# Kernel optimization log

Hardware: AMD Instinct MI355X
Metric: run time of the kernel (lower is better)

The kernel has to match this reference:

```python
import jax, jax.numpy as jnp
import numpy as np

HID = 768
INNER = 1536   # hidden_size * expand_factor
NSTATE = 16
KCONV = 4
EPS = 1e-5


def _layernorm(x, w, b):
    mu = jnp.mean(x, axis=-1, keepdims=True)
    var = jnp.mean(jnp.square(x - mu), axis=-1, keepdims=True)
    return (x - mu) * jax.lax.rsqrt(var + EPS) * w + b


def setup_inputs() -> dict:
    key = jax.random.key(0)
    ks = jax.random.split(key, 8)
    B, S = 2, 2048
    s_in = 1.0 / np.sqrt(HID).astype(np.float32)
    s_inner = 1.0 / np.sqrt(INNER).astype(np.float32)
    s_k = 1.0 / np.sqrt(KCONV).astype(np.float32)
    return {
        "x": jax.random.normal(ks[0], (B, S, HID), jnp.float32),
        "norm_w": jnp.ones((HID,), jnp.float32),
        "norm_b": jnp.zeros((HID,), jnp.float32),
        "W_in": jax.random.normal(ks[1], (HID, 2 * INNER), jnp.float32) * s_in,
        "conv_w": jax.random.normal(ks[2], (INNER, 1, KCONV), jnp.float32) * s_k,  # OIH depthwise
        "W_xproj": jax.random.normal(ks[3], (INNER, 2 * NSTATE + INNER), jnp.float32) * s_inner,
        "A_log": jax.random.normal(ks[4], (NSTATE,), jnp.float32),
        "D": jnp.ones((INNER,), jnp.float32),
        "W_ssm_out": jax.random.normal(ks[5], (INNER, INNER), jnp.float32) * s_inner,
        "W_out": jax.random.normal(ks[6], (INNER, HID), jnp.float32) * s_inner,
    }


def _selective_ssm(u, W_xproj, A_log, D, W_ssm_out):
    # u: (B, S, INNER)
    proj = u @ W_xproj                                   # (B,S,2N+INNER)
    Bm = proj[..., :NSTATE]                              # (B,S,N)
    Cm = proj[..., NSTATE:2 * NSTATE]                    # (B,S,N)
    delta = jax.nn.softplus(proj[..., 2 * NSTATE:])      # (B,S,INNER)
    A = -jnp.exp(A_log)                                  # (N,)

    def step(h, inp):
        d_t, b_t, c_t, u_t = inp                          # (B,INNER),(B,N),(B,N),(B,INNER)
        dA = jnp.exp(d_t[:, None, :] * A[None, :, None])  # (B,N,INNER)
        h = dA * h + (d_t * u_t)[:, None, :] * b_t[:, :, None]
        y = jnp.einsum('bnh,bn->bh', h, c_t)
        return h, y

    B_, S_, _ = u.shape
    h0 = jnp.zeros((B_, NSTATE, INNER), u.dtype)
    xs = (jnp.moveaxis(delta, 1, 0), jnp.moveaxis(Bm, 1, 0),
          jnp.moveaxis(Cm, 1, 0), jnp.moveaxis(u, 1, 0))
    _, ys = jax.lax.scan(step, h0, xs)                   # (S,B,INNER)
    y = jnp.moveaxis(ys, 0, 1) + D * u
    return y @ W_ssm_out


def reference(x, norm_w, norm_b, W_in, conv_w, W_xproj, A_log, D, W_ssm_out, W_out):
    residual = x
    xn = _layernorm(x, norm_w, norm_b)
    xp = xn @ W_in                                       # (B,S,2*INNER)
    u, gate = jnp.split(xp, 2, axis=-1)
    # causal depthwise conv1d (torch pads k-1 both sides then truncates -> left pad k-1)
    uc = jax.lax.conv_general_dilated(
        jnp.swapaxes(u, 1, 2), conv_w, window_strides=(1,),
        padding=[(KCONV - 1, 0)], dimension_numbers=('NCH', 'OIH', 'NCH'),
        feature_group_count=INNER)
    u = jax.nn.silu(jnp.swapaxes(uc, 1, 2))              # (B,S,INNER)
    y = _selective_ssm(u, W_xproj, A_log, D, W_ssm_out)
    y = y * jax.nn.silu(gate)
    out = y @ W_out + residual                           # dropout is identity in eval
    return out
```

## Files before the change

kernel.cpp:

```cpp
#include <hip/hip_runtime.h>
#include <cstdint>
#include <cmath>

#define HID 768
#define INNER 1536
#define NST 16
#define SEQ 2048
#define BATCH 2
#define MTOK 4096
#define CHUNK 32
#define NCHUNK 64
#define LOG2E 1.44269504088896f

typedef unsigned short u16;
typedef __bf16 bf16x8 __attribute__((ext_vector_type(8)));
typedef float f32x4 __attribute__((ext_vector_type(4)));
typedef u16 u16x8 __attribute__((ext_vector_type(8)));

__device__ __forceinline__ u16 f2b(float f) {
  union { float f; unsigned u; } a; a.f = f;
  unsigned r = a.u + 0x7FFFu + ((a.u >> 16) & 1u);
  return (u16)(r >> 16);
}
__device__ __forceinline__ float b2f(u16 h) {
  union { unsigned u; float f; } a; a.u = ((unsigned)h) << 16; return a.f;
}

__device__ __forceinline__ long pidx(long m, int k, int KS) {
  return (((m >> 4) * (long)KS + (k >> 5)) * 64 + ((k >> 3) & 3) * 16 + (m & 15)) * 8 + (k & 7);
}

__global__ __launch_bounds__(256)
void ln_kernel(const float* __restrict__ x, const float* __restrict__ w,
               const float* __restrict__ b, u16* __restrict__ xnp) {
  const long row = blockIdx.x;
  const float* xr = x + row * HID;
  const int t = threadIdx.x;
  float v0 = xr[t], v1 = xr[t + 256], v2 = xr[t + 512];
  float s1 = v0 + v1 + v2;
  float s2 = v0 * v0 + v1 * v1 + v2 * v2;
#pragma unroll
  for (int o = 32; o > 0; o >>= 1) { s1 += __shfl_down(s1, o); s2 += __shfl_down(s2, o); }
  __shared__ float r1[4], r2[4];
  if ((t & 63) == 0) { r1[t >> 6] = s1; r2[t >> 6] = s2; }
  __syncthreads();
  s1 = r1[0] + r1[1] + r1[2] + r1[3];
  s2 = r2[0] + r2[1] + r2[2] + r2[3];
  const float mu = s1 * (1.f / HID);
  float var = s2 * (1.f / HID) - mu * mu;
  const float rs = rsqrtf(var + 1e-5f);
  xnp[pidx(row, t,       24)] = f2b((v0 - mu) * rs * w[t]       + b[t]);
  xnp[pidx(row, t + 256, 24)] = f2b((v1 - mu) * rs * w[t + 256] + b[t + 256]);
  xnp[pidx(row, t + 512, 24)] = f2b((v2 - mu) * rs * w[t + 512] + b[t + 512]);
}

__global__ __launch_bounds__(256)
void pack_w(const float* __restrict__ W, u16* __restrict__ Bp, int K, int N) {
  __shared__ float tb[32][65];
  const int t = threadIdx.x;
  const int n0 = blockIdx.x * 64;
  const int ks = blockIdx.y;
  const int k0 = ks * 32;
  const int KS = K >> 5;
  {
    const int col = t & 63, row0 = t >> 6;
    const int nn = n0 + col;
#pragma unroll
    for (int rr = 0; rr < 8; ++rr) {
      const int kk = k0 + row0 + rr * 4;
      tb[row0 + rr * 4][col] = (nn < N) ? W[(long)kk * N + nn] : 0.f;
    }
  }
  __syncthreads();
  const int ntl = t >> 6, l4 = (t >> 4) & 3, l16 = t & 15;
  const int nl = ntl * 16 + l16;
  u16x8 outv;
#pragma unroll
  for (int wdx = 0; wdx < 8; ++wdx) outv[wdx] = f2b(tb[l4 * 8 + wdx][nl]);
  const long tile = (n0 >> 4) + ntl;
  *(u16x8*)&Bp[(tile * KS + ks) * 512 + (l4 * 16 + l16) * 8] = outv;
}

template <int FI, int FJ, int NBLK, int EPI>
__global__ __launch_bounds__(256)
void gemm_pk(const u16* __restrict__ Ap, const u16* __restrict__ Bp,
             float* __restrict__ O0, float* __restrict__ O1, u16* __restrict__ O2,
             const float* __restrict__ Ef, const u16* __restrict__ Eb,
             int K, int Nstore) {
  constexpr int WM = 256 / FI;
  constexpr int PERX = WM / 16;
  const int KS = K >> 5;
  const int u = blockIdx.x;
  const int wave = threadIdx.x >> 6;
  const int lane = threadIdx.x & 63;
  const int xcd = u & 7;
  const int s = u >> 3;
  const int wmrow = (xcd * PERX + s / NBLK) * 2 + (wave >> 1);
  const int wn = (s % NBLK) * 2 + (wave & 1);

  const u16* a0 = Ap + ((long)(wmrow * FI) * KS * 64 + lane) * 8;
  const u16* b0 = Bp + ((long)(wn * FJ) * KS * 64 + lane) * 8;

  f32x4 acc[FI][FJ] = {};
  bf16x8 afA[FI], bfA[FJ], afB[FI], bfB[FJ];

#pragma unroll
  for (int i = 0; i < FI; ++i) afA[i] = *(const bf16x8*)(a0 + (long)i * KS * 512);
#pragma unroll
  for (int j = 0; j < FJ; ++j) bfA[j] = *(const bf16x8*)(b0 + (long)j * KS * 512);

  for (int ks = 0; ks < KS; ks += 2) {
#pragma unroll
    for (int i = 0; i < FI; ++i) afB[i] = *(const bf16x8*)(a0 + ((long)i * KS + ks + 1) * 512);
#pragma unroll
    for (int j = 0; j < FJ; ++j) bfB[j] = *(const bf16x8*)(b0 + ((long)j * KS + ks + 1) * 512);
#pragma unroll
    for (int i = 0; i < FI; ++i)
#pragma unroll
      for (int j = 0; j < FJ; ++j)
        acc[i][j] = __builtin_amdgcn_mfma_f32_16x16x32_bf16(afA[i], bfA[j], acc[i][j], 0, 0, 0);
    if (ks + 2 < KS) {
#pragma unroll
      for (int i = 0; i < FI; ++i) afA[i] = *(const bf16x8*)(a0 + ((long)i * KS + ks + 2) * 512);
#pragma unroll
      for (int j = 0; j < FJ; ++j) bfA[j] = *(const bf16x8*)(b0 + ((long)j * KS + ks + 2) * 512);
    }
#pragma unroll
    for (int i = 0; i < FI; ++i)
#pragma unroll
      for (int j = 0; j < FJ; ++j)
        acc[i][j] = __builtin_amdgcn_mfma_f32_16x16x32_bf16(afB[i], bfB[j], acc[i][j], 0, 0, 0);
  }

  const int l16 = lane & 15, l4 = lane >> 4;
#pragma unroll
  for (int i = 0; i < FI; ++i) {
    const long rr = (long)(wmrow * FI + i) * 16 + l4 * 4;
#pragma unroll
    for (int j = 0; j < FJ; ++j) {
      const int cc = (wn * FJ + j) * 16 + l16;
#pragma unroll
      for (int r = 0; r < 4; ++r) {
        const long row = rr + r;
        const float v = acc[i][j][r];
        if (EPI == 0) {
          if (cc < 1536) O0[row * 1536 + cc] = v;
          else {
            float sv = v / (1.f + __expf(-v));
            O2[row * 1536 + (cc - 1536)] = f2b(sv);
          }
        } else if (EPI == 1) {
          if (cc < 16) O0[row * 16 + cc] = v;
          else if (cc < 32) O1[row * 16 + (cc - 16)] = v;
          else if (cc < Nstore) {
            float sp = (v > 20.f) ? v : log1pf(__expf(v));
            O2[row * 1536 + (cc - 32)] = f2b(sp);
          }
        } else if (EPI == 2) {
          float g = b2f(Eb[row * 1536 + cc]);
          O2[pidx(row, cc, 48)] = f2b(v * g);
        } else {
          O0[row * 768 + cc] = v + Ef[row * 768 + cc];
        }
      }
    }
  }
}

__global__ __launch_bounds__(256)
void conv_silu(const float* __restrict__ xpu, const float* __restrict__ cw,
               u16* __restrict__ ub, u16* __restrict__ ubp) {
  const int c = blockIdx.x * 256 + threadIdx.x;
  const long m = blockIdx.y;
  const int t = (int)(m & (SEQ - 1));
  const float w0 = cw[c * 4 + 0], w1 = cw[c * 4 + 1], w2 = cw[c * 4 + 2], w3 = cw[c * 4 + 3];
  float acc = w3 * xpu[m * 1536 + c];
  if (t >= 1) acc += w2 * xpu[(m - 1) * 1536 + c];
  if (t >= 2) acc += w1 * xpu[(m - 2) * 1536 + c];
  if (t >= 3) acc += w0 * xpu[(m - 3) * 1536 + c];
  const float s = acc / (1.f + __expf(-acc));
  const u16 sb = f2b(s);
  ub[m * 1536 + c] = sb;
  ubp[pidx(m, c, 48)] = sb;
}

__global__ __launch_bounds__(256)
void scan_phaseA(const u16* __restrict__ dlt, const u16* __restrict__ ub,
                 const float* __restrict__ Bm, const float* __restrict__ A_log,
                 float* __restrict__ P, float* __restrict__ Q) {
  const int tid = threadIdx.x;
  const int cl = tid >> 2;
  const int sg = tid & 3;
  const int c = blockIdx.x * 64 + cl;
  const int b = blockIdx.y;
  const int ch = blockIdx.z;
  float a2[4];
#pragma unroll
  for (int j = 0; j < 4; ++j) a2[j] = -__expf(A_log[sg * 4 + j]) * LOG2E;
  float h[4] = {0.f, 0.f, 0.f, 0.f};
  float sumd = 0.f;
  const long base = (long)b * SEQ + (long)ch * CHUNK;
  for (int t = 0; t < CHUNK; ++t) {
    const long m = base + t;
    const float d = b2f(dlt[m * 1536 + c]);
    const float du = d * b2f(ub[m * 1536 + c]);
    sumd += d;
    const f32x4 Bv = *(const f32x4*)&Bm[m * 16 + sg * 4];
#pragma unroll
    for (int j = 0; j < 4; ++j) {
      const float e = exp2f(a2[j] * d);
      h[j] = e * h[j] + du * Bv[j];
    }
  }
  const long sb = (((long)b * NCHUNK + ch) * NST + sg * 4) * 1536 + c;
#pragma unroll
  for (int j = 0; j < 4; ++j) {
    Q[sb + (long)j * 1536] = h[j];
    P[sb + (long)j * 1536] = exp2f(a2[j] * sumd);
  }
}

__global__ __launch_bounds__(256)
void scan_phaseB(float* __restrict__ P, const float* __restrict__ Q) {
  const long g = (long)blockIdx.x * 256 + threadIdx.x;
  const int c = (int)(g % 1536);
  const int n = (int)((g / 1536) % NST);
  const int b = (int)(g / (1536 * NST));
  float h = 0.f;
  for (int ch = 0; ch < NCHUNK; ++ch) {
    const long idx = (((long)b * NCHUNK + ch) * NST + n) * 1536 + c;
    const float p = P[idx];
    const float q = Q[idx];
    P[idx] = h;
    h = p * h + q;
  }
}

__global__ __launch_bounds__(256)
void scan_phaseC(const u16* __restrict__ dlt, const u16* __restrict__ ub,
                 const float* __restrict__ Bm, const float* __restrict__ Cm,
                 const float* __restrict__ A_log, const float* __restrict__ Dv,
                 const float* __restrict__ hs, u16* __restrict__ ysp) {
  const int tid = threadIdx.x;
  const int cl = tid >> 2;
  const int sg = tid & 3;
  const int c = blockIdx.x * 64 + cl;
  const int b = blockIdx.y;
  const int ch = blockIdx.z;
  float a2[4];
#pragma unroll
  for (int j = 0; j < 4; ++j) a2[j] = -__expf(A_log[sg * 4 + j]) * LOG2E;
  float h[4];
  const long sb = (((long)b * NCHUNK + ch) * NST + sg * 4) * 1536 + c;
#pragma unroll
  for (int j = 0; j < 4; ++j) h[j] = hs[sb + (long)j * 1536];
  const float Dc = Dv[c];
  const long base = (long)b * SEQ + (long)ch * CHUNK;
  for (int t = 0; t < CHUNK; ++t) {
    const long m = base + t;
    const float d = b2f(dlt[m * 1536 + c]);
    const float uu = b2f(ub[m * 1536 + c]);
    const float du = d * uu;
    const f32x4 Bv = *(const f32x4*)&Bm[m * 16 + sg * 4];
    const f32x4 Cv = *(const f32x4*)&Cm[m * 16 + sg * 4];
    float y = (sg == 0) ? Dc * uu : 0.f;
#pragma unroll
    for (int j = 0; j < 4; ++j) {
      const float e = exp2f(a2[j] * d);
      h[j] = e * h[j] + du * Bv[j];
      y += h[j] * Cv[j];
    }
    y += __shfl_xor(y, 1);
    y += __shfl_xor(y, 2);
    if (sg == 0) ysp[pidx(m, c, 48)] = f2b(y);
  }
}

extern "C" void kernel_launch(void* const* d_in, const int* in_sizes, int n_in,
                              void* d_out, int out_size, void* d_ws, size_t ws_size,
                              hipStream_t stream) {
  const float* x     = (const float*)d_in[0];
  const float* nw    = (const float*)d_in[1];
  const float* nb    = (const float*)d_in[2];
  const float* W_in  = (const float*)d_in[3];
  const float* cw    = (const float*)d_in[4];
  const float* W_xp  = (const float*)d_in[5];
  const float* A_log = (const float*)d_in[6];
  const float* Dv    = (const float*)d_in[7];
  const float* W_so  = (const float*)d_in[8];
  const float* W_out = (const float*)d_in[9];
  float* out = (float*)d_out;

  char* w = (char*)d_ws;
  auto alloc = [&](size_t bytes) {
    char* p = w;
    w += (bytes + 255) & ~(size_t)255;
    return p;
  };
  u16*   xnp   = (u16*)  alloc((size_t)MTOK * HID * 2);
  u16*   WpIn  = (u16*)  alloc((size_t)3072 * 768 * 2);
  float* xpu   = (float*)alloc((size_t)MTOK * 1536 * 4);
  u16*   sg    = (u16*)  alloc((size_t)MTOK * 1536 * 2);
  u16*   ub    = (u16*)  alloc((size_t)MTOK * 1536 * 2);
  u16*   ubp   = (u16*)  alloc((size_t)MTOK * 1536 * 2);
  u16*   WpXp  = (u16*)  alloc((size_t)1664 * 1536 * 2);
  float* Bmv   = (float*)alloc((size_t)MTOK * 16 * 4);
  float* Cmv   = (float*)alloc((size_t)MTOK * 16 * 4);
  u16*   dlt   = (u16*)  alloc((size_t)MTOK * 1536 * 2);
  float* P     = (float*)alloc((size_t)BATCH * NCHUNK * NST * 1536 * 4);
  float* Q     = (float*)alloc((size_t)BATCH * NCHUNK * NST * 1536 * 4);
  u16*   ysp   = (u16*)  alloc((size_t)MTOK * 1536 * 2);
  u16*   WpSo  = (u16*)  alloc((size_t)1536 * 1536 * 2);
  u16*   zbp   = (u16*)  alloc((size_t)MTOK * 1536 * 2);
  u16*   WpOut = (u16*)  alloc((size_t)768 * 1536 * 2);

  ln_kernel<<<MTOK, 256, 0, stream>>>(x, nw, nb, xnp);
  pack_w<<<dim3(48, 24), 256, 0, stream>>>(W_in,  WpIn,  768,  3072);
  pack_w<<<dim3(26, 48), 256, 0, stream>>>(W_xp,  WpXp,  1536, 1568);
  pack_w<<<dim3(24, 48), 256, 0, stream>>>(W_so,  WpSo,  1536, 1536);
  pack_w<<<dim3(12, 48), 256, 0, stream>>>(W_out, WpOut, 1536, 768);

  gemm_pk<4, 4, 24, 0><<<768, 256, 0, stream>>>(xnp, WpIn, xpu, nullptr, sg, nullptr, nullptr, 768, 3072);
  conv_silu<<<dim3(6, MTOK), 256, 0, stream>>>(xpu, cw, ub, ubp);
  gemm_pk<4, 2, 26, 1><<<832, 256, 0, stream>>>(ubp, WpXp, Bmv, Cmv, dlt, nullptr, nullptr, 1536, 1568);
  scan_phaseA<<<dim3(24, 2, NCHUNK), 256, 0, stream>>>(dlt, ub, Bmv, A_log, P, Q);
  scan_phaseB<<<192, 256, 0, stream>>>(P, Q);
  scan_phaseC<<<dim3(24, 2, NCHUNK), 256, 0, stream>>>(dlt, ub, Bmv, Cmv, A_log, Dv, P, ysp);
  gemm_pk<4, 2, 24, 2><<<768, 256, 0, stream>>>(ysp, WpSo, nullptr, nullptr, zbp, nullptr, sg, 1536, 1536);
  gemm_pk<2, 2, 12, 3><<<768, 256, 0, stream>>>(zbp, WpOut, out, nullptr, nullptr, x, nullptr, 1536, 768);
}
```

Baseline: 408.3 us.

## Triple-buffer GEMM register fragments and split in-proj GEMM into more blocks

The packed MFMA GEMM main loop now keeps three register fragment sets in flight instead of two, with per-fragment pointers that advance by three K-steps per iteration. This deepens the global-load prefetch so more memory latency is hidden behind the MFMA work. The input-projection GEMM also changes from 4x4 to 4x2 fragments per wave and launches twice as many blocks, giving more parallelism at the cost of less reuse per block. The loop assumes KS is divisible by 3, which holds for K=768 and K=1536. Triple buffering also raises register pressure.

```diff
diff --git a/kernel.cpp b/kernel.cpp
--- a/kernel.cpp
+++ b/kernel.cpp
@@ -98,39 +98,53 @@
   const int wmrow = (xcd * PERX + s / NBLK) * 2 + (wave >> 1);
   const int wn = (s % NBLK) * 2 + (wave & 1);
 
-  const u16* a0 = Ap + ((long)(wmrow * FI) * KS * 64 + lane) * 8;
-  const u16* b0 = Bp + ((long)(wn * FJ) * KS * 64 + lane) * 8;
+  const u16* pa[FI];
+  const u16* pb[FJ];
+#pragma unroll
+  for (int i = 0; i < FI; ++i)
+    pa[i] = Ap + ((long)(wmrow * FI + i) * KS * 64 + lane) * 8;
+#pragma unroll
+  for (int j = 0; j < FJ; ++j)
+    pb[j] = Bp + ((long)(wn * FJ + j) * KS * 64 + lane) * 8;
 
   f32x4 acc[FI][FJ] = {};
-  bf16x8 afA[FI], bfA[FJ], afB[FI], bfB[FJ];
-
-#pragma unroll
-  for (int i = 0; i < FI; ++i) afA[i] = *(const bf16x8*)(a0 + (long)i * KS * 512);
-#pragma unroll
-  for (int j = 0; j < FJ; ++j) bfA[j] = *(const bf16x8*)(b0 + (long)j * KS * 512);
-
-  for (int ks = 0; ks < KS; ks += 2) {
-#pragma unroll
-    for (int i = 0; i < FI; ++i) afB[i] = *(const bf16x8*)(a0 + ((long)i * KS + ks + 1) * 512);
-#pragma unroll
-    for (int j = 0; j < FJ; ++j) bfB[j] = *(const bf16x8*)(b0 + ((long)j * KS + ks + 1) * 512);
+  bf16x8 fa0[FI], fa1[FI], fa2[FI], fb0[FJ], fb1[FJ], fb2[FJ];
+
+  auto rld = [&](bf16x8 (&A)[FI], bf16x8 (&B)[FJ], int off) {
+#pragma unroll
+    for (int i = 0; i < FI; ++i) A[i] = *(const bf16x8*)(pa[i] + off);
+#pragma unroll
+    for (int j = 0; j < FJ; ++j) B[j] = *(const bf16x8*)(pb[j] + off);
+  };
+  auto comp = [&](bf16x8 (&A)[FI], bf16x8 (&B)[FJ]) {
 #pragma unroll
     for (int i = 0; i < FI; ++i)
 #pragma unroll
       for (int j = 0; j < FJ; ++j)
-        acc[i][j] = __builtin_amdgcn_mfma_f32_16x16x32_bf16(afA[i], bfA[j], acc[i][j], 0, 0, 0);
-    if (ks + 2 < KS) {
-#pragma unroll
-      for (int i = 0; i < FI; ++i) afA[i] = *(const bf16x8*)(a0 + ((long)i * KS + ks + 2) * 512);
-#pragma unroll
-      for (int j = 0; j < FJ; ++j) bfA[j] = *(const bf16x8*)(b0 + ((long)j * KS + ks + 2) * 512);
-    }
-#pragma unroll
-    for (int i = 0; i < FI; ++i)
-#pragma unroll
-      for (int j = 0; j < FJ; ++j)
-        acc[i][j] = __builtin_amdgcn_mfma_f32_16x16x32_bf16(afB[i], bfB[j], acc[i][j], 0, 0, 0);
-  }
+        acc[i][j] = __builtin_amdgcn_mfma_f32_16x16x32_bf16(A[i], B[j], acc[i][j], 0, 0, 0);
+  };
+  auto bump = [&]() {
+#pragma unroll
+    for (int i = 0; i < FI; ++i) pa[i] += 1536;
+#pragma unroll
+    for (int j = 0; j < FJ; ++j) pb[j] += 1536;
+  };
+
+  rld(fa0, fb0, 0);
+  rld(fa1, fb1, 512);
+  rld(fa2, fb2, 1024);
+  bump();
+
+  const int iters = KS / 3 - 1;
+  for (int it = 0; it < iters; ++it) {
+    comp(fa0, fb0); rld(fa0, fb0, 0);
+    comp(fa1, fb1); rld(fa1, fb1, 512);
+    comp(fa2, fb2); rld(fa2, fb2, 1024);
+    bump();
+  }
+  comp(fa0, fb0);
+  comp(fa1, fb1);
+  comp(fa2, fb2);
 
   const int l16 = lane & 15, l4 = lane >> 4;
 #pragma unroll
@@ -320,7 +334,7 @@
   pack_w<<<dim3(24, 48), 256, 0, stream>>>(W_so,  WpSo,  1536, 1536);
   pack_w<<<dim3(12, 48), 256, 0, stream>>>(W_out, WpOut, 1536, 768);
 
-  gemm_pk<4, 4, 24, 0><<<768, 256, 0, stream>>>(xnp, WpIn, xpu, nullptr, sg, nullptr, nullptr, 768, 3072);
+  gemm_pk<4, 2, 48, 0><<<1536, 256, 0, stream>>>(xnp, WpIn, xpu, nullptr, sg, nullptr, nullptr, 768, 3072);
   conv_silu<<<dim3(6, MTOK), 256, 0, stream>>>(xpu, cw, ub, ubp);
   gemm_pk<4, 2, 26, 1><<<832, 256, 0, stream>>>(ubp, WpXp, Bmv, Cmv, dlt, nullptr, nullptr, 1536, 1568);
   scan_phaseA<<<dim3(24, 2, NCHUNK), 256, 0, stream>>>(dlt, ub, Bmv, A_log, P, Q);
```

Measured after the change: 401.3 us. About the same (-1.7%).

## Stage GEMM tiles through double-buffered LDS with 128x128 block tiles

Applied to the files above, without the earlier changes.

Replaces the register-direct GEMM, where each wave loaded its own A/B fragments from global memory, with a block-level 128x128 tile staged through double-buffered shared memory. The four waves share the A and B fragments, which cuts redundant global loads, and the next k-slice load overlaps the current MFMAs. The first projection's u-half output is also stored as bf16 instead of fp32, halving its write and the conv kernel's read at some cost in precision. Grids get smaller (for example 192 blocks for the output GEMM), which can lower occupancy across the GPU's compute units.

```diff
diff --git a/kernel.cpp b/kernel.cpp
--- a/kernel.cpp
+++ b/kernel.cpp
@@ -81,86 +81,99 @@
   *(u16x8*)&Bp[(tile * KS + ks) * 512 + (l4 * 16 + l16) * 8] = outv;
 }
 
-template <int FI, int FJ, int NBLK, int EPI>
-__global__ __launch_bounds__(256)
-void gemm_pk(const u16* __restrict__ Ap, const u16* __restrict__ Bp,
-             float* __restrict__ O0, float* __restrict__ O1, u16* __restrict__ O2,
+template <int NBX, int EPI>
+__global__ __launch_bounds__(256, 3)
+void gemm_db(const u16* __restrict__ Ap, const u16* __restrict__ Bp,
+             float* __restrict__ F0, float* __restrict__ F1,
+             u16* __restrict__ U0, u16* __restrict__ U1,
              const float* __restrict__ Ef, const u16* __restrict__ Eb,
              int K, int Nstore) {
-  constexpr int WM = 256 / FI;
-  constexpr int PERX = WM / 16;
   const int KS = K >> 5;
+  __shared__ uint4 lds[2][1024];
+  const int tid = threadIdx.x;
+  const int wave = tid >> 6, lane = tid & 63;
+  const int chunk = tid >> 4, part = tid & 15;
   const int u = blockIdx.x;
-  const int wave = threadIdx.x >> 6;
-  const int lane = threadIdx.x & 63;
-  const int xcd = u & 7;
-  const int s = u >> 3;
-  const int wmrow = (xcd * PERX + s / NBLK) * 2 + (wave >> 1);
-  const int wn = (s % NBLK) * 2 + (wave & 1);
-
-  const u16* a0 = Ap + ((long)(wmrow * FI) * KS * 64 + lane) * 8;
-  const u16* b0 = Bp + ((long)(wn * FJ) * KS * 64 + lane) * 8;
-
-  f32x4 acc[FI][FJ] = {};
-  bf16x8 afA[FI], bfA[FJ], afB[FI], bfB[FJ];
-
-#pragma unroll
-  for (int i = 0; i < FI; ++i) afA[i] = *(const bf16x8*)(a0 + (long)i * KS * 512);
-#pragma unroll
-  for (int j = 0; j < FJ; ++j) bfA[j] = *(const bf16x8*)(b0 + (long)j * KS * 512);
-
-  for (int ks = 0; ks < KS; ks += 2) {
-#pragma unroll
-    for (int i = 0; i < FI; ++i) afB[i] = *(const bf16x8*)(a0 + ((long)i * KS + ks + 1) * 512);
-#pragma unroll
-    for (int j = 0; j < FJ; ++j) bfB[j] = *(const bf16x8*)(b0 + ((long)j * KS + ks + 1) * 512);
-#pragma unroll
-    for (int i = 0; i < FI; ++i)
-#pragma unroll
-      for (int j = 0; j < FJ; ++j)
-        acc[i][j] = __builtin_amdgcn_mfma_f32_16x16x32_bf16(afA[i], bfA[j], acc[i][j], 0, 0, 0);
-    if (ks + 2 < KS) {
-#pragma unroll
-      for (int i = 0; i < FI; ++i) afA[i] = *(const bf16x8*)(a0 + ((long)i * KS + ks + 2) * 512);
-#pragma unroll
-      for (int j = 0; j < FJ; ++j) bfA[j] = *(const bf16x8*)(b0 + ((long)j * KS + ks + 2) * 512);
-    }
-#pragma unroll
-    for (int i = 0; i < FI; ++i)
-#pragma unroll
-      for (int j = 0; j < FJ; ++j)
-        acc[i][j] = __builtin_amdgcn_mfma_f32_16x16x32_bf16(afB[i], bfB[j], acc[i][j], 0, 0, 0);
+  const int xcd = u & 7, s = u >> 3;
+  const int bmt = xcd * 4 + s / NBX;
+  const int bnt = s % NBX;
+
+  const long tile = (chunk < 8) ? (long)(bmt * 8 + chunk) : (long)(bnt * 8 + (chunk - 8));
+  const uint4* src = (const uint4*)((chunk < 8 ? Ap : Bp) + tile * (long)KS * 512) + part * 4;
+  const int ldsoff = chunk * 64 + part * 4;
+
+  uint4 ra[4], rb[4];
+  auto loadg = [&](uint4 (&r)[4], int kk) {
+    const uint4* p = src + (long)kk * 64;
+#pragma unroll
+    for (int q = 0; q < 4; ++q) r[q] = p[q];
+  };
+  auto writes = [&](uint4 (&r)[4], int b) {
+#pragma unroll
+    for (int q = 0; q < 4; ++q) lds[b][ldsoff + q] = r[q];
+  };
+
+  f32x4 acc[4][4] = {};
+  const int wm = wave >> 1, wn = wave & 1;
+
+  loadg(ra, 0);
+  loadg(rb, 1);
+  writes(ra, 0);
+  __builtin_amdgcn_s_waitcnt(0xC07F);
+  __builtin_amdgcn_s_barrier();
+
+  for (int k = 0; k < KS; ++k) {
+    const int cur = k & 1;
+    const bool even = (k & 1) == 0;
+    if (k + 2 < KS) loadg(even ? ra : rb, k + 2);
+    bf16x8 af[4], bfv[4];
+#pragma unroll
+    for (int i = 0; i < 4; ++i)
+      af[i] = *(const bf16x8*)&lds[cur][(wm * 4 + i) * 64 + lane];
+#pragma unroll
+    for (int j = 0; j < 4; ++j)
+      bfv[j] = *(const bf16x8*)&lds[cur][(8 + wn * 4 + j) * 64 + lane];
+    if (k + 1 < KS) {
+      writes(even ? rb : ra, cur ^ 1);
+      __builtin_amdgcn_s_waitcnt(0xC07F);
+      __builtin_amdgcn_s_barrier();
+    }
+#pragma unroll
+    for (int i = 0; i < 4; ++i)
+#pragma unroll
+      for (int j = 0; j < 4; ++j)
+        acc[i][j] = __builtin_amdgcn_mfma_f32_16x16x32_bf16(af[i], bfv[j], acc[i][j], 0, 0, 0);
   }
 
   const int l16 = lane & 15, l4 = lane >> 4;
 #pragma unroll
-  for (int i = 0; i < FI; ++i) {
-    const long rr = (long)(wmrow * FI + i) * 16 + l4 * 4;
-#pragma unroll
-    for (int j = 0; j < FJ; ++j) {
-      const int cc = (wn * FJ + j) * 16 + l16;
+  for (int i = 0; i < 4; ++i) {
+    const long rr = (long)bmt * 128 + (wm * 4 + i) * 16 + l4 * 4;
+#pragma unroll
+    for (int j = 0; j < 4; ++j) {
+      const int cc = bnt * 128 + (wn * 4 + j) * 16 + l16;
 #pragma unroll
       for (int r = 0; r < 4; ++r) {
         const long row = rr + r;
         const float v = acc[i][j][r];
         if (EPI == 0) {
-          if (cc < 1536) O0[row * 1536 + cc] = v;
+          if (cc < 1536) U0[row * 1536 + cc] = f2b(v);
           else {
             float sv = v / (1.f + __expf(-v));
-            O2[row * 1536 + (cc - 1536)] = f2b(sv);
+            U1[row * 1536 + (cc - 1536)] = f2b(sv);
           }
         } else if (EPI == 1) {
-          if (cc < 16) O0[row * 16 + cc] = v;
-          else if (cc < 32) O1[row * 16 + (cc - 16)] = v;
+          if (cc < 16) F0[row * 16 + cc] = v;
+          else if (cc < 32) F1[row * 16 + (cc - 16)] = v;
           else if (cc < Nstore) {
             float sp = (v > 20.f) ? v : log1pf(__expf(v));
-            O2[row * 1536 + (cc - 32)] = f2b(sp);
+            U0[row * 1536 + (cc - 32)] = f2b(sp);
           }
         } else if (EPI == 2) {
           float g = b2f(Eb[row * 1536 + cc]);
-          O2[pidx(row, cc, 48)] = f2b(v * g);
+          U0[pidx(row, cc, 48)] = f2b(v * g);
         } else {
-          O0[row * 768 + cc] = v + Ef[row * 768 + cc];
+          F0[row * 768 + cc] = v + Ef[row * 768 + cc];
         }
       }
     }
@@ -168,16 +181,16 @@
 }
 
 __global__ __launch_bounds__(256)
-void conv_silu(const float* __restrict__ xpu, const float* __restrict__ cw,
+void conv_silu(const u16* __restrict__ xpub, const float* __restrict__ cw,
                u16* __restrict__ ub, u16* __restrict__ ubp) {
   const int c = blockIdx.x * 256 + threadIdx.x;
   const long m = blockIdx.y;
   const int t = (int)(m & (SEQ - 1));
   const float w0 = cw[c * 4 + 0], w1 = cw[c * 4 + 1], w2 = cw[c * 4 + 2], w3 = cw[c * 4 + 3];
-  float acc = w3 * xpu[m * 1536 + c];
-  if (t >= 1) acc += w2 * xpu[(m - 1) * 1536 + c];
-  if (t >= 2) acc += w1 * xpu[(m - 2) * 1536 + c];
-  if (t >= 3) acc += w0 * xpu[(m - 3) * 1536 + c];
+  float acc = w3 * b2f(xpub[m * 1536 + c]);
+  if (t >= 1) acc += w2 * b2f(xpub[(m - 1) * 1536 + c]);
+  if (t >= 2) acc += w1 * b2f(xpub[(m - 2) * 1536 + c]);
+  if (t >= 3) acc += w0 * b2f(xpub[(m - 3) * 1536 + c]);
   const float s = acc / (1.f + __expf(-acc));
   const u16 sb = f2b(s);
   ub[m * 1536 + c] = sb;
@@ -299,7 +312,7 @@
   };
   u16*   xnp   = (u16*)  alloc((size_t)MTOK * HID * 2);
   u16*   WpIn  = (u16*)  alloc((size_t)3072 * 768 * 2);
-  float* xpu   = (float*)alloc((size_t)MTOK * 1536 * 4);
+  u16*   xpub  = (u16*)  alloc((size_t)MTOK * 1536 * 2);
   u16*   sg    = (u16*)  alloc((size_t)MTOK * 1536 * 2);
   u16*   ub    = (u16*)  alloc((size_t)MTOK * 1536 * 2);
   u16*   ubp   = (u16*)  alloc((size_t)MTOK * 1536 * 2);
@@ -320,12 +333,12 @@
   pack_w<<<dim3(24, 48), 256, 0, stream>>>(W_so,  WpSo,  1536, 1536);
   pack_w<<<dim3(12, 48), 256, 0, stream>>>(W_out, WpOut, 1536, 768);
 
-  gemm_pk<4, 4, 24, 0><<<768, 256, 0, stream>>>(xnp, WpIn, xpu, nullptr, sg, nullptr, nullptr, 768, 3072);
-  conv_silu<<<dim3(6, MTOK), 256, 0, stream>>>(xpu, cw, ub, ubp);
-  gemm_pk<4, 2, 26, 1><<<832, 256, 0, stream>>>(ubp, WpXp, Bmv, Cmv, dlt, nullptr, nullptr, 1536, 1568);
+  gemm_db<24, 0><<<768, 256, 0, stream>>>(xnp, WpIn, nullptr, nullptr, xpub, sg, nullptr, nullptr, 768, 3072);
+  conv_silu<<<dim3(6, MTOK), 256, 0, stream>>>(xpub, cw, ub, ubp);
+  gemm_db<13, 1><<<416, 256, 0, stream>>>(ubp, WpXp, Bmv, Cmv, dlt, nullptr, nullptr, nullptr, 1536, 1568);
   scan_phaseA<<<dim3(24, 2, NCHUNK), 256, 0, stream>>>(dlt, ub, Bmv, A_log, P, Q);
   scan_phaseB<<<192, 256, 0, stream>>>(P, Q);
   scan_phaseC<<<dim3(24, 2, NCHUNK), 256, 0, stream>>>(dlt, ub, Bmv, Cmv, A_log, Dv, P, ysp);
-  gemm_pk<4, 2, 24, 2><<<768, 256, 0, stream>>>(ysp, WpSo, nullptr, nullptr, zbp, nullptr, sg, 1536, 1536);
-  gemm_pk<2, 2, 12, 3><<<768, 256, 0, stream>>>(zbp, WpOut, out, nullptr, nullptr, x, nullptr, 1536, 768);
-}
+  gemm_db<12, 2><<<384, 256, 0, stream>>>(ysp, WpSo, nullptr, nullptr, zbp, nullptr, nullptr, sg, 1536, 1536);
+  gemm_db<6, 3><<<192, 256, 0, stream>>>(zbp, WpOut, out, nullptr, nullptr, nullptr, x, nullptr, 1536, 768);
+}
```

Result: slower. 661.8 us (+62.1%).
